# Optimization experiments

Hardware: AMD Instinct MI355X
Metric: run time of the kernel (lower is better)

Reference implementation:

```python
import jax, jax.numpy as jnp
import numpy as np

N_NODES = 10000
N_EDGES = 150000
N_GRAPHS = 64
D_IN = 128
D_HID = 512  # 2**9 hard-coded in the module
D_OUT = 128


def setup_inputs() -> dict:
    key = jax.random.key(0)
    ks = jax.random.split(key, 16)
    x = jax.random.normal(ks[0], (N_NODES, D_IN), dtype=jnp.float32)
    edge_index = jax.random.randint(ks[1], (2, N_EDGES), 0, N_NODES, dtype=jnp.int32)
    batch = jnp.sort(jax.random.randint(ks[2], (N_NODES,), 0, N_GRAPHS, dtype=jnp.int32))
    dims = [(D_IN, D_HID), (D_HID, D_HID), (D_HID, D_HID), (D_HID, D_HID), (D_HID, D_OUT)]
    params = {}
    for i, (fi, fo) in enumerate(dims):
        scale = 1.0 / np.sqrt(fi)
        params[f"W{i+1}"] = jax.random.uniform(ks[3 + 2 * i], (fi, fo), jnp.float32, -scale, scale)
        params[f"b{i+1}"] = jnp.zeros((fo,), jnp.float32)
    return {"x": x, "edge_index": edge_index, "batch": batch, **params}


def reference(x, edge_index, batch, W1, b1, W2, b2, W3, b3, W4, b4, W5, b5):
    N = x.shape[0]
    # GCNConv: add self-loops, symmetric normalization D^-1/2 (A+I) D^-1/2
    loop = jnp.arange(N, dtype=edge_index.dtype)
    src = jnp.concatenate([edge_index[0], loop])  # message sources
    dst = jnp.concatenate([edge_index[1], loop])  # aggregation targets
    deg = jax.ops.segment_sum(jnp.ones_like(dst, x.dtype), dst, num_segments=N)
    dinv = jnp.where(deg > 0, jax.lax.rsqrt(deg), 0.0)
    norm = (dinv[src] * dinv[dst])[:, None]  # [E+N, 1]

    def gcn_conv(h, W, b):
        hW = h @ W                              # dense GEMM [N, fo]
        msg = hW[src] * norm                    # gather + edgewise scale
        return jax.ops.segment_sum(msg, dst, num_segments=N) + b

    h = jax.nn.relu(gcn_conv(x, W1, b1))
    h = jax.nn.relu(gcn_conv(h, W2, b2))
    h = jax.nn.relu(gcn_conv(h, W3, b3))
    h = jax.nn.relu(gcn_conv(h, W4, b4))
    h = jax.nn.relu(gcn_conv(h, W5, b5))

    # global_mean_pool over graph ids
    sums = jax.ops.segment_sum(h, batch, num_segments=N_GRAPHS)
    cnts = jax.ops.segment_sum(jnp.ones((N,), h.dtype), batch, num_segments=N_GRAPHS)
    return sums / jnp.maximum(cnts, 1.0)[:, None]
```

## Files before the change

kernel.cpp:

```cpp
#include <hip/hip_runtime.h>
#include <stdint.h>

#define NN 10000
#define NE 150000
#define NG 64
#define DIN 128
#define DHID 512
#define DOUT 128
#define POOL_P 16

typedef float f32x4 __attribute__((ext_vector_type(4)));
typedef short s16x8 __attribute__((ext_vector_type(8)));
typedef unsigned short us4 __attribute__((ext_vector_type(4)));
typedef unsigned short us2 __attribute__((ext_vector_type(2)));
typedef unsigned short ushort_t;

__device__ __forceinline__ ushort_t f2bf(float f) {
    unsigned u = __float_as_uint(f);
    u += 0x7FFFu + ((u >> 16) & 1u);
    return (ushort_t)(u >> 16);
}
__device__ __forceinline__ float bf2f(ushort_t s) {
    return __uint_as_float(((unsigned)s) << 16);
}

__device__ __forceinline__ void gl_lds16(const void* g, void* l) {
    __builtin_amdgcn_global_load_lds(
        (const __attribute__((address_space(1))) unsigned int*)g,
        (__attribute__((address_space(3))) unsigned int*)l, 16, 0, 0);
}

__device__ __forceinline__ void mfma_bf16(f32x4& d, s16x8 a, s16x8 b) {
    asm("v_mfma_f32_16x16x32_bf16 %0, %1, %2, %0" : "+v"(d) : "v"(a), "v"(b));
}

__global__ void k_edges_count(const int* __restrict__ dst, int* __restrict__ cnt, int E) {
    int e = blockIdx.x * blockDim.x + threadIdx.x;
    if (e < E) atomicAdd(&cnt[dst[e]], 1);
}

__global__ void k_dinv(const int* __restrict__ cnt, float* __restrict__ dinv, int n) {
    int i = blockIdx.x * blockDim.x + threadIdx.x;
    if (i < n) dinv[i] = rsqrtf(1.0f + (float)cnt[i]);
}

__global__ void k_scan2(const int* __restrict__ cnt, int* __restrict__ rp) {
    const int C = 10;
    const int t = threadIdx.x;
    const int lane = t & 63, w = t >> 6;
    const int base = t * C;
    int v[C];
    int s = 0;
#pragma unroll
    for (int j = 0; j < C; j++) {
        int i = base + j;
        v[j] = (i < NN) ? cnt[i] : 0;
        s += v[j];
    }
    int sc = s;
#pragma unroll
    for (int off = 1; off < 64; off <<= 1) {
        int tv = __shfl_up(sc, off);
        if (lane >= off) sc += tv;
    }
    __shared__ int wsum[16], woff[16];
    if (lane == 63) wsum[w] = sc;
    __syncthreads();
    if (t == 0) {
        int c = 0;
#pragma unroll
        for (int k = 0; k < 16; k++) { woff[k] = c; c += wsum[k]; }
    }
    __syncthreads();
    int pre = woff[w] + (sc - s);
#pragma unroll
    for (int j = 0; j < C; j++) {
        int i = base + j;
        if (i <= NN) rp[i] = pre;
        pre += v[j];
    }
}

__global__ void k_scatter(const int* __restrict__ src, const int* __restrict__ dst,
                          const float* __restrict__ dinv, const int* __restrict__ rp,
                          int* __restrict__ fill, int* __restrict__ es,
                          float* __restrict__ ew, int E) {
    int e = blockIdx.x * blockDim.x + threadIdx.x;
    if (e < E) {
        int d = dst[e], s = src[e];
        int p = rp[d] + atomicAdd(&fill[d], 1);
        es[p] = s;
        ew[p] = dinv[s] * dinv[d];
    }
}

__global__ void k_split_w(const float* __restrict__ W1, const float* __restrict__ W2,
                          const float* __restrict__ W3, const float* __restrict__ W4,
                          const float* __restrict__ W5,
                          ushort_t* __restrict__ th, ushort_t* __restrict__ tl) {
    int t = blockIdx.x * blockDim.x + threadIdx.x;
    const float* W;
    int K, Mw, off, r;
    if (t < 65536)       { W = W1; K = 128; Mw = 512; off = 0;      r = t; }
    else if (t < 327680) { W = W2; K = 512; Mw = 512; off = 65536;  r = t - 65536; }
    else if (t < 589824) { W = W3; K = 512; Mw = 512; off = 327680; r = t - 327680; }
    else if (t < 851968) { W = W4; K = 512; Mw = 512; off = 589824; r = t - 589824; }
    else if (t < 917504) { W = W5; K = 512; Mw = 128; off = 851968; r = t - 851968; }
    else return;
    const int k = r / Mw, m = r % Mw;
    const float f = W[r];
    const ushort_t h = f2bf(f);
    const ushort_t l = f2bf(f - bf2f(h));
    const int o = off + m * K + k;
    th[o] = h;
    tl[o] = l;
}

template <int EPI>
__global__ __launch_bounds__(256, 2) void k_mgemm(
    const ushort_t* __restrict__ Ah, const ushort_t* __restrict__ Al,
    const ushort_t* __restrict__ Bh, const ushort_t* __restrict__ Bl,
    const float* __restrict__ bias,
    ushort_t* __restrict__ Ch, ushort_t* __restrict__ Cl, float* __restrict__ Cf,
    const int M, const int N, const int K) {
    __shared__ ushort_t sAh[128 * 32], sAl[128 * 32], sBh[128 * 32], sBl[128 * 32];
    const int tid = threadIdx.x;
    const int lane = tid & 63, wv = tid >> 6;
    const int ln = lane & 15, lhi = lane >> 4;
    const int kg = lhi * 8;
    const int wr = (wv >> 1) * 64, wc = (wv & 1) * 64;
    const int row0 = blockIdx.y * 128, col0 = blockIdx.x * 128;
    const int sr = tid >> 2;
    const int sk = (tid & 3) * 8;

    f32x4 acc[4][4] = {};

    for (int k0 = 0; k0 < K; k0 += 32) {
        __syncthreads();
        {
            const int koff = k0 + sk;
            int ra0 = row0 + sr;      if (ra0 > M - 1) ra0 = M - 1;
            int ra1 = row0 + 64 + sr; if (ra1 > M - 1) ra1 = M - 1;
            gl_lds16(&Ah[(size_t)ra0 * K + koff], &sAh[sr * 32 + sk]);
            gl_lds16(&Ah[(size_t)ra1 * K + koff], &sAh[(64 + sr) * 32 + sk]);
            gl_lds16(&Al[(size_t)ra0 * K + koff], &sAl[sr * 32 + sk]);
            gl_lds16(&Al[(size_t)ra1 * K + koff], &sAl[(64 + sr) * 32 + sk]);
            const size_t cb0 = (size_t)(col0 + sr) * K + koff;
            const size_t cb1 = (size_t)(col0 + 64 + sr) * K + koff;
            gl_lds16(&Bh[cb0], &sBh[sr * 32 + sk]);
            gl_lds16(&Bh[cb1], &sBh[(64 + sr) * 32 + sk]);
            gl_lds16(&Bl[cb0], &sBl[sr * 32 + sk]);
            gl_lds16(&Bl[cb1], &sBl[(64 + sr) * 32 + sk]);
        }
        __syncthreads();

        s16x8 a_h[4], a_l[4], b_h[4], b_l[4];
#pragma unroll
        for (int m = 0; m < 4; m++) {
            const int r = (wr + m * 16 + ln) * 32 + kg;
            a_h[m] = *reinterpret_cast<const s16x8*>(&sAh[r]);
            a_l[m] = *reinterpret_cast<const s16x8*>(&sAl[r]);
        }
#pragma unroll
        for (int n = 0; n < 4; n++) {
            const int c = (wc + n * 16 + ln) * 32 + kg;
            b_h[n] = *reinterpret_cast<const s16x8*>(&sBh[c]);
            b_l[n] = *reinterpret_cast<const s16x8*>(&sBl[c]);
        }
#pragma unroll
        for (int m = 0; m < 4; m++)
#pragma unroll
            for (int n = 0; n < 4; n++) {
                mfma_bf16(acc[m][n], a_h[m], b_h[n]);
                mfma_bf16(acc[m][n], a_h[m], b_l[n]);
                mfma_bf16(acc[m][n], a_l[m], b_h[n]);
            }
    }

    asm volatile("s_nop 7\n\ts_nop 7");

#pragma unroll
    for (int n = 0; n < 4; n++) {
        const int col = col0 + wc + n * 16 + ln;
        const float bv = (EPI == 2) ? bias[col] : 0.0f;
#pragma unroll
        for (int m = 0; m < 4; m++) {
#pragma unroll
            for (int j = 0; j < 4; j++) {
                const int row = row0 + wr + m * 16 + lhi * 4 + j;
                if (row < M) {
                    float f = acc[m][n][j];
                    const size_t o = (size_t)row * N + col;
                    if constexpr (EPI == 2) {
                        f = fmaxf(f + bv, 0.0f);
                        const ushort_t h = f2bf(f);
                        Ch[o] = h;
                        Cl[o] = f2bf(f - bf2f(h));
                    } else {
                        Cf[o] = f;
                    }
                }
            }
        }
    }
}

template <int M_, int TPB, int OUTM>
__global__ void k_agg(const float* __restrict__ xf, const float* __restrict__ dinv,
                      const int* __restrict__ rp, const int* __restrict__ es,
                      const float* __restrict__ ew, const float* __restrict__ bias,
                      float* __restrict__ of, ushort_t* __restrict__ oh,
                      ushort_t* __restrict__ ol) {
    constexpr int VEC = M_ / TPB;
    static_assert(VEC == 2 || VEC == 4, "");
    const int node = blockIdx.x;
    const int tid = threadIdx.x;
    __shared__ int s_src[64];
    __shared__ float s_w[64];

    const float di = dinv[node];
    const float sw = di * di;
    const size_t selfo = (size_t)node * M_ + tid * VEC;
    float acc[VEC];
    if constexpr (VEC == 4) {
        float4 v = *reinterpret_cast<const float4*>(&xf[selfo]);
        acc[0] = v.x * sw; acc[1] = v.y * sw; acc[2] = v.z * sw; acc[3] = v.w * sw;
    } else {
        float2 v = *reinterpret_cast<const float2*>(&xf[selfo]);
        acc[0] = v.x * sw; acc[1] = v.y * sw;
    }

    const int beg = rp[node], end = rp[node + 1];
    for (int c = beg; c < end; c += 64) {
        const int m = min(64, end - c);
        __syncthreads();
        if (tid < m) { s_src[tid] = es[c + tid]; s_w[tid] = ew[c + tid]; }
        __syncthreads();
        for (int e = 0; e < m; e++) {
            const float w = s_w[e];
            const size_t o = (size_t)s_src[e] * M_ + tid * VEC;
            if constexpr (VEC == 4) {
                float4 v = *reinterpret_cast<const float4*>(&xf[o]);
                acc[0] = fmaf(v.x, w, acc[0]); acc[1] = fmaf(v.y, w, acc[1]);
                acc[2] = fmaf(v.z, w, acc[2]); acc[3] = fmaf(v.w, w, acc[3]);
            } else {
                float2 v = *reinterpret_cast<const float2*>(&xf[o]);
                acc[0] = fmaf(v.x, w, acc[0]); acc[1] = fmaf(v.y, w, acc[1]);
            }
        }
    }

#pragma unroll
    for (int j = 0; j < VEC; j++) {
        float f = acc[j];
        if constexpr (OUTM != 1) f = fmaxf(f + bias[tid * VEC + j], 0.0f);
        acc[j] = f;
    }
    if constexpr (OUTM == 0) {
        if constexpr (VEC == 4)
            *reinterpret_cast<float4*>(&of[selfo]) = make_float4(acc[0], acc[1], acc[2], acc[3]);
        else
            *reinterpret_cast<float2*>(&of[selfo]) = make_float2(acc[0], acc[1]);
    } else {
        ushort_t hh[VEC], ll[VEC];
#pragma unroll
        for (int j = 0; j < VEC; j++) {
            hh[j] = f2bf(acc[j]);
            ll[j] = f2bf(acc[j] - bf2f(hh[j]));
        }
        if constexpr (VEC == 4) {
            us4 h4 = {hh[0], hh[1], hh[2], hh[3]}, l4 = {ll[0], ll[1], ll[2], ll[3]};
            *reinterpret_cast<us4*>(&oh[selfo]) = h4;
            *reinterpret_cast<us4*>(&ol[selfo]) = l4;
        } else {
            us2 h2 = {hh[0], hh[1]}, l2 = {ll[0], ll[1]};
            *reinterpret_cast<us2*>(&oh[selfo]) = h2;
            *reinterpret_cast<us2*>(&ol[selfo]) = l2;
        }
    }
}

__global__ void k_gbounds(const int* __restrict__ batch, int* __restrict__ gstart) {
    const int g = threadIdx.x;
    if (g > NG) return;
    int lo = 0, hi = NN;
    while (lo < hi) {
        int mid = (lo + hi) >> 1;
        if (batch[mid] < g) lo = mid + 1; else hi = mid;
    }
    gstart[g] = lo;
}

__global__ void k_pool_part(const float* __restrict__ h, const int* __restrict__ gstart,
                            float* __restrict__ partial) {
    const int g = blockIdx.x, p = blockIdx.y;
    const int f = threadIdx.x;
    const int s = gstart[g], e = gstart[g + 1];
    const int len = e - s;
    const int chunk = (len + POOL_P - 1) / POOL_P;
    const int i0 = s + p * chunk;
    const int i1 = min(i0 + chunk, e);
    float a0 = 0.f, a1 = 0.f, a2 = 0.f, a3 = 0.f;
    int i = i0;
    for (; i + 3 < i1; i += 4) {
        a0 += h[(size_t)(i + 0) * DOUT + f];
        a1 += h[(size_t)(i + 1) * DOUT + f];
        a2 += h[(size_t)(i + 2) * DOUT + f];
        a3 += h[(size_t)(i + 3) * DOUT + f];
    }
    for (; i < i1; i++) a0 += h[(size_t)i * DOUT + f];
    partial[(size_t)(g * POOL_P + p) * DOUT + f] = (a0 + a1) + (a2 + a3);
}

__global__ void k_pool_fin(const float* __restrict__ partial, const int* __restrict__ gstart,
                           float* __restrict__ out) {
    const int g = blockIdx.x;
    const int f = threadIdx.x;
    float acc = 0.f;
#pragma unroll
    for (int p = 0; p < POOL_P; p++) acc += partial[(size_t)(g * POOL_P + p) * DOUT + f];
    const float cnt = (float)(gstart[g + 1] - gstart[g]);
    out[(size_t)g * DOUT + f] = acc / fmaxf(cnt, 1.0f);
}

extern "C" void kernel_launch(void* const* d_in, const int* in_sizes, int n_in,
                              void* d_out, int out_size, void* d_ws, size_t ws_size,
                              hipStream_t stream) {
    const float* x = (const float*)d_in[0];
    const int* ei = (const int*)d_in[1];
    const int* batch = (const int*)d_in[2];
    const float* b1 = (const float*)d_in[4];
    const float* b2 = (const float*)d_in[6];
    const float* b3 = (const float*)d_in[8];
    const float* b4 = (const float*)d_in[10];
    const float* b5 = (const float*)d_in[12];
    const int* src = ei;
    const int* dst = ei + NE;

    char* ws = (char*)d_ws;
    size_t off = 0;
    auto alloc = [&](size_t bytes) -> char* {
        char* p = ws + off;
        off = (off + bytes + 255) & ~(size_t)255;
        return p;
    };
    float* dinv = (float*)alloc(NN * 4);
    int* cnt    = (int*)alloc(NN * 4);
    int* rp     = (int*)alloc((NN + 1) * 4);
    int* fill   = (int*)alloc(NN * 4);
    int* es     = (int*)alloc(NE * 4);
    float* ewn  = (float*)alloc(NE * 4);
    int* gstart = (int*)alloc((NG + 1) * 4);
    float* ppart = (float*)alloc((size_t)NG * POOL_P * DOUT * 4);
    ushort_t* wth = (ushort_t*)alloc(917504 * 2);
    ushort_t* wtl = (ushort_t*)alloc(917504 * 2);
    ushort_t* Xh = (ushort_t*)alloc((size_t)NN * DHID * 2);
    ushort_t* Xl = (ushort_t*)alloc((size_t)NN * DHID * 2);
    ushort_t* Yh = (ushort_t*)alloc((size_t)NN * DHID * 2);
    ushort_t* Yl = (ushort_t*)alloc((size_t)NN * DHID * 2);
    float* hF = (float*)alloc((size_t)NN * DHID * 4);
    float* hOut = (float*)Xh;
    (void)ws_size; (void)n_in; (void)in_sizes;

    hipMemsetAsync(cnt, 0, NN * 4, stream);
    hipMemsetAsync(fill, 0, NN * 4, stream);

    k_edges_count<<<(NE + 255) / 256, 256, 0, stream>>>(dst, cnt, NE);
    k_dinv<<<(NN + 255) / 256, 256, 0, stream>>>(cnt, dinv, NN);
    k_scan2<<<1, 1024, 0, stream>>>(cnt, rp);
    k_scatter<<<(NE + 255) / 256, 256, 0, stream>>>(src, dst, dinv, rp, fill, es, ewn, NE);
    k_gbounds<<<1, 128, 0, stream>>>(batch, gstart);

    k_split_w<<<(917504 + 255) / 256, 256, 0, stream>>>(
        (const float*)d_in[3], (const float*)d_in[5], (const float*)d_in[7],
        (const float*)d_in[9], (const float*)d_in[11], wth, wtl);

    const int gy = (NN + 127) / 128;
    const ushort_t *w1h = wth, *w1l = wtl;
    const ushort_t *w2h = wth + 65536, *w2l = wtl + 65536;
    const ushort_t *w3h = wth + 327680, *w3l = wtl + 327680;
    const ushort_t *w4h = wth + 589824, *w4l = wtl + 589824;
    const ushort_t *w5h = wth + 851968, *w5l = wtl + 851968;

    k_agg<DIN, 64, 1><<<NN, 64, 0, stream>>>(x, dinv, rp, es, ewn, nullptr,
                                             nullptr, Xh, Xl);
    k_mgemm<2><<<dim3(4, gy), 256, 0, stream>>>(Xh, Xl, w1h, w1l, b1, Yh, Yl, nullptr,
                                                NN, DHID, DIN);

    k_mgemm<0><<<dim3(4, gy), 256, 0, stream>>>(Yh, Yl, w2h, w2l, nullptr, nullptr, nullptr, hF,
                                                NN, DHID, DHID);
    k_agg<DHID, 128, 2><<<NN, 128, 0, stream>>>(hF, dinv, rp, es, ewn, b2, nullptr, Yh, Yl);
    k_mgemm<0><<<dim3(4, gy), 256, 0, stream>>>(Yh, Yl, w3h, w3l, nullptr, nullptr, nullptr, hF,
                                                NN, DHID, DHID);
    k_agg<DHID, 128, 2><<<NN, 128, 0, stream>>>(hF, dinv, rp, es, ewn, b3, nullptr, Yh, Yl);
    k_mgemm<0><<<dim3(4, gy), 256, 0, stream>>>(Yh, Yl, w4h, w4l, nullptr, nullptr, nullptr, hF,
                                                NN, DHID, DHID);
    k_agg<DHID, 128, 2><<<NN, 128, 0, stream>>>(hF, dinv, rp, es, ewn, b4, nullptr, Yh, Yl);

    k_mgemm<0><<<dim3(1, gy), 256, 0, stream>>>(Yh, Yl, w5h, w5l, nullptr, nullptr, nullptr, hF,
                                                NN, DOUT, DHID);
    k_agg<DOUT, 64, 0><<<NN, 64, 0, stream>>>(hF, dinv, rp, es, ewn, b5, hOut, nullptr, nullptr);

    k_pool_part<<<dim3(NG, POOL_P), DOUT, 0, stream>>>(hOut, gstart, ppart);
    k_pool_fin<<<NG, DOUT, 0, stream>>>(ppart, gstart, (float*)d_out);
}
```

Before: 416.7 us.

## Double-buffer GEMM LDS tiles and unroll aggregation gathers with split accumulators

```diff
diff --git a/kernel.cpp b/kernel.cpp
--- a/kernel.cpp
+++ b/kernel.cpp
@@ -123,7 +123,8 @@
     const float* __restrict__ bias,
     ushort_t* __restrict__ Ch, ushort_t* __restrict__ Cl, float* __restrict__ Cf,
     const int M, const int N, const int K) {
-    __shared__ ushort_t sAh[128 * 32], sAl[128 * 32], sBh[128 * 32], sBl[128 * 32];
+    __shared__ ushort_t sAh[2][128 * 32], sAl[2][128 * 32];
+    __shared__ ushort_t sBh[2][128 * 32], sBl[2][128 * 32];
     const int tid = threadIdx.x;
     const int lane = tid & 63, wv = tid >> 6;
     const int ln = lane & 15, lhi = lane >> 4;
@@ -133,39 +134,44 @@
     const int sr = tid >> 2;
     const int sk = (tid & 3) * 8;
 
+    auto STAGE = [&](int buf, int k0) {
+        const int koff = k0 + sk;
+        int ra0 = row0 + sr;      if (ra0 > M - 1) ra0 = M - 1;
+        int ra1 = row0 + 64 + sr; if (ra1 > M - 1) ra1 = M - 1;
+        gl_lds16(&Ah[(size_t)ra0 * K + koff], &sAh[buf][sr * 32 + sk]);
+        gl_lds16(&Ah[(size_t)ra1 * K + koff], &sAh[buf][(64 + sr) * 32 + sk]);
+        gl_lds16(&Al[(size_t)ra0 * K + koff], &sAl[buf][sr * 32 + sk]);
+        gl_lds16(&Al[(size_t)ra1 * K + koff], &sAl[buf][(64 + sr) * 32 + sk]);
+        const size_t cb0 = (size_t)(col0 + sr) * K + koff;
+        const size_t cb1 = (size_t)(col0 + 64 + sr) * K + koff;
+        gl_lds16(&Bh[cb0], &sBh[buf][sr * 32 + sk]);
+        gl_lds16(&Bh[cb1], &sBh[buf][(64 + sr) * 32 + sk]);
+        gl_lds16(&Bl[cb0], &sBl[buf][sr * 32 + sk]);
+        gl_lds16(&Bl[cb1], &sBl[buf][(64 + sr) * 32 + sk]);
+    };
+
     f32x4 acc[4][4] = {};
 
-    for (int k0 = 0; k0 < K; k0 += 32) {
-        __syncthreads();
-        {
-            const int koff = k0 + sk;
-            int ra0 = row0 + sr;      if (ra0 > M - 1) ra0 = M - 1;
-            int ra1 = row0 + 64 + sr; if (ra1 > M - 1) ra1 = M - 1;
-            gl_lds16(&Ah[(size_t)ra0 * K + koff], &sAh[sr * 32 + sk]);
-            gl_lds16(&Ah[(size_t)ra1 * K + koff], &sAh[(64 + sr) * 32 + sk]);
-            gl_lds16(&Al[(size_t)ra0 * K + koff], &sAl[sr * 32 + sk]);
-            gl_lds16(&Al[(size_t)ra1 * K + koff], &sAl[(64 + sr) * 32 + sk]);
-            const size_t cb0 = (size_t)(col0 + sr) * K + koff;
-            const size_t cb1 = (size_t)(col0 + 64 + sr) * K + koff;
-            gl_lds16(&Bh[cb0], &sBh[sr * 32 + sk]);
-            gl_lds16(&Bh[cb1], &sBh[(64 + sr) * 32 + sk]);
-            gl_lds16(&Bl[cb0], &sBl[sr * 32 + sk]);
-            gl_lds16(&Bl[cb1], &sBl[(64 + sr) * 32 + sk]);
-        }
-        __syncthreads();
+    STAGE(0, 0);
+    __syncthreads();
+
+    const int nk = K / 32;
+    for (int t = 0; t < nk; t++) {
+        const int cur = t & 1;
+        if (t + 1 < nk) STAGE(cur ^ 1, (t + 1) * 32);
 
         s16x8 a_h[4], a_l[4], b_h[4], b_l[4];
 #pragma unroll
         for (int m = 0; m < 4; m++) {
             const int r = (wr + m * 16 + ln) * 32 + kg;
-            a_h[m] = *reinterpret_cast<const s16x8*>(&sAh[r]);
-            a_l[m] = *reinterpret_cast<const s16x8*>(&sAl[r]);
+            a_h[m] = *reinterpret_cast<const s16x8*>(&sAh[cur][r]);
+            a_l[m] = *reinterpret_cast<const s16x8*>(&sAl[cur][r]);
         }
 #pragma unroll
         for (int n = 0; n < 4; n++) {
             const int c = (wc + n * 16 + ln) * 32 + kg;
-            b_h[n] = *reinterpret_cast<const s16x8*>(&sBh[c]);
-            b_l[n] = *reinterpret_cast<const s16x8*>(&sBl[c]);
+            b_h[n] = *reinterpret_cast<const s16x8*>(&sBh[cur][c]);
+            b_l[n] = *reinterpret_cast<const s16x8*>(&sBl[cur][c]);
         }
 #pragma unroll
         for (int m = 0; m < 4; m++)
@@ -175,6 +181,7 @@
                 mfma_bf16(acc[m][n], a_h[m], b_l[n]);
                 mfma_bf16(acc[m][n], a_l[m], b_h[n]);
             }
+        __syncthreads();
     }
 
     asm volatile("s_nop 7\n\ts_nop 7");
@@ -221,13 +228,13 @@
     const float di = dinv[node];
     const float sw = di * di;
     const size_t selfo = (size_t)node * M_ + tid * VEC;
-    float acc[VEC];
+    float a0[VEC], a1[VEC] = {}, a2[VEC] = {}, a3[VEC] = {};
     if constexpr (VEC == 4) {
         float4 v = *reinterpret_cast<const float4*>(&xf[selfo]);
-        acc[0] = v.x * sw; acc[1] = v.y * sw; acc[2] = v.z * sw; acc[3] = v.w * sw;
+        a0[0] = v.x * sw; a0[1] = v.y * sw; a0[2] = v.z * sw; a0[3] = v.w * sw;
     } else {
         float2 v = *reinterpret_cast<const float2*>(&xf[selfo]);
-        acc[0] = v.x * sw; acc[1] = v.y * sw;
+        a0[0] = v.x * sw; a0[1] = v.y * sw;
     }
 
     const int beg = rp[node], end = rp[node + 1];
@@ -236,37 +243,69 @@
         __syncthreads();
         if (tid < m) { s_src[tid] = es[c + tid]; s_w[tid] = ew[c + tid]; }
         __syncthreads();
-        for (int e = 0; e < m; e++) {
+        int e = 0;
+        for (; e + 3 < m; e += 4) {
+            const float w0 = s_w[e], w1 = s_w[e + 1], w2 = s_w[e + 2], w3 = s_w[e + 3];
+            const size_t o0 = (size_t)s_src[e] * M_ + tid * VEC;
+            const size_t o1 = (size_t)s_src[e + 1] * M_ + tid * VEC;
+            const size_t o2 = (size_t)s_src[e + 2] * M_ + tid * VEC;
+            const size_t o3 = (size_t)s_src[e + 3] * M_ + tid * VEC;
+            if constexpr (VEC == 4) {
+                float4 v0 = *reinterpret_cast<const float4*>(&xf[o0]);
+                float4 v1 = *reinterpret_cast<const float4*>(&xf[o1]);
+                float4 v2 = *reinterpret_cast<const float4*>(&xf[o2]);
+                float4 v3 = *reinterpret_cast<const float4*>(&xf[o3]);
+                a0[0] = fmaf(v0.x, w0, a0[0]); a0[1] = fmaf(v0.y, w0, a0[1]);
+                a0[2] = fmaf(v0.z, w0, a0[2]); a0[3] = fmaf(v0.w, w0, a0[3]);
+                a1[0] = fmaf(v1.x, w1, a1[0]); a1[1] = fmaf(v1.y, w1, a1[1]);
+                a1[2] = fmaf(v1.z, w1, a1[2]); a1[3] = fmaf(v1.w, w1, a1[3]);
+                a2[0] = fmaf(v2.x, w2, a2[0]); a2[1] = fmaf(v2.y, w2, a2[1]);
+                a2[2] = fmaf(v2.z, w2, a2[2]); a2[3] = fmaf(v2.w, w2, a2[3]);
+                a3[0] = fmaf(v3.x, w3, a3[0]); a3[1] = fmaf(v3.y, w3, a3[1]);
+                a3[2] = fmaf(v3.z, w3, a3[2]); a3[3] = fmaf(v3.w, w3, a3[3]);
+            } else {
+                float2 v0 = *reinterpret_cast<const float2*>(&xf[o0]);
+                float2 v1 = *reinterpret_cast<const float2*>(&xf[o1]);
+                float2 v2 = *reinterpret_cast<const float2*>(&xf[o2]);
+                float2 v3 = *reinterpret_cast<const float2*>(&xf[o3]);
+                a0[0] = fmaf(v0.x, w0, a0[0]); a0[1] = fmaf(v0.y, w0, a0[1]);
+                a1[0] = fmaf(v1.x, w1, a1[0]); a1[1] = fmaf(v1.y, w1, a1[1]);
+                a2[0] = fmaf(v2.x, w2, a2[0]); a2[1] = fmaf(v2.y, w2, a2[1]);
+                a3[0] = fmaf(v3.x, w3, a3[0]); a3[1] = fmaf(v3.y, w3, a3[1]);
+            }
+        }
+        for (; e < m; e++) {
             const float w = s_w[e];
             const size_t o = (size_t)s_src[e] * M_ + tid * VEC;
             if constexpr (VEC == 4) {
                 float4 v = *reinterpret_cast<const float4*>(&xf[o]);
-                acc[0] = fmaf(v.x, w, acc[0]); acc[1] = fmaf(v.y, w, acc[1]);
-                acc[2] = fmaf(v.z, w, acc[2]); acc[3] = fmaf(v.w, w, acc[3]);
+                a0[0] = fmaf(v.x, w, a0[0]); a0[1] = fmaf(v.y, w, a0[1]);
+                a0[2] = fmaf(v.z, w, a0[2]); a0[3] = fmaf(v.w, w, a0[3]);
             } else {
                 float2 v = *reinterpret_cast<const float2*>(&xf[o]);
-                acc[0] = fmaf(v.x, w, acc[0]); acc[1] = fmaf(v.y, w, acc[1]);
+                a0[0] = fmaf(v.x, w, a0[0]); a0[1] = fmaf(v.y, w, a0[1]);
             }
         }
     }
 
+    float accv[VEC];
 #pragma unroll
     for (int j = 0; j < VEC; j++) {
-        float f = acc[j];
+        float f = (a0[j] + a1[j]) + (a2[j] + a3[j]);
         if constexpr (OUTM != 1) f = fmaxf(f + bias[tid * VEC + j], 0.0f);
-        acc[j] = f;
+        accv[j] = f;
     }
     if constexpr (OUTM == 0) {
         if constexpr (VEC == 4)
-            *reinterpret_cast<float4*>(&of[selfo]) = make_float4(acc[0], acc[1], acc[2], acc[3]);
+            *reinterpret_cast<float4*>(&of[selfo]) = make_float4(accv[0], accv[1], accv[2], accv[3]);
         else
-            *reinterpret_cast<float2*>(&of[selfo]) = make_float2(acc[0], acc[1]);
+            *reinterpret_cast<float2*>(&of[selfo]) = make_float2(accv[0], accv[1]);
     } else {
         ushort_t hh[VEC], ll[VEC];
 #pragma unroll
         for (int j = 0; j < VEC; j++) {
-            hh[j] = f2bf(acc[j]);
-            ll[j] = f2bf(acc[j] - bf2f(hh[j]));
+            hh[j] = f2bf(accv[j]);
+            ll[j] = f2bf(accv[j] - bf2f(hh[j]));
         }
         if constexpr (VEC == 4) {
             us4 h4 = {hh[0], hh[1], hh[2], hh[3]}, l4 = {ll[0], ll[1], ll[2], ll[3]};
```

New measurement: 415.4 us. Within noise of the previous version (-0.3%).
